# Kernel optimization log

Measured on AMD Instinct MI355X. Metric: run time of the kernel, lower is better.

The kernel has to match this reference:

```python
import jax, jax.numpy as jnp
import numpy as np

N_NODES = 100000
N_EDGES = 1250000
D = 64
K = 5
EPS = 1e-8


def setup_inputs() -> dict:
    key = jax.random.key(0)
    k1, k2, k3, k4 = jax.random.split(key, 4)
    x = jax.random.normal(k1, (N_NODES, D), dtype=jnp.float32)
    mask = jax.random.normal(k2, (N_NODES, 1), dtype=jnp.float32)
    edge_index = jax.random.randint(k3, (2, N_EDGES), 0, N_NODES, dtype=jnp.int64)
    # orthogonal-ish init for the linear layer (QR of gaussian), gain for tanh = 5/3
    g = jax.random.normal(k4, (D, D), dtype=jnp.float32)
    q, _ = jnp.linalg.qr(g)
    W = (5.0 / 3.0) * q.astype(jnp.float32)
    b = jnp.zeros((D,), dtype=jnp.float32)
    alpha = jnp.float32(0.001)
    return {"x": x, "mask": mask, "edge_index": edge_index, "W": W, "b": b, "alpha": alpha}


def _forward(x, mask, edge_index, W, b, alpha):
    n = x.shape[0]
    # x_fn: Linear + Tanh
    h = jnp.tanh(x @ W.T + b)  # [N, D]
    src = edge_index[0]
    dst = edge_index[1]
    hs = h[src]  # [E, D] gather
    hd = h[dst]  # [E, D] gather
    # torch cosine_similarity with eps clamp on each norm
    ns = jnp.maximum(jnp.sqrt(jnp.sum(hs * hs, axis=-1)), EPS)
    nd = jnp.maximum(jnp.sqrt(jnp.sum(hd * hd, axis=-1)), EPS)
    cos = jnp.sum(hs * hd, axis=-1) / (ns * nd)
    edge_weights = jax.nn.relu(cos)  # [E]

    # gcn_norm with self loops (PyG APPNP default): D^-1/2 (A + I) D^-1/2
    loop = jnp.arange(n, dtype=src.dtype)
    row = jnp.concatenate([src, loop])
    col = jnp.concatenate([dst, loop])
    w = jnp.concatenate([edge_weights, jnp.ones((n,), dtype=edge_weights.dtype)])
    deg = jax.ops.segment_sum(w, col, num_segments=n)
    dis = jnp.where(deg > 0, jax.lax.rsqrt(jnp.maximum(deg, EPS)), 0.0)
    norm_w = dis[row] * w * dis[col]  # [E + N]

    # APPNP: K steps of f = (1-alpha) * A_hat @ f + alpha * f0
    f0 = jax.nn.relu(mask)  # [N, 1]
    f = f0
    for _ in range(K):
        msg = norm_w[:, None] * f[row]  # gather + weight
        agg = jax.ops.segment_sum(msg, col, num_segments=n)  # scatter-add
        f = (1.0 - alpha) * agg + alpha * f0
    return f, edge_weights


def reference(x, mask, edge_index, W, b, alpha):
    return _forward(x, mask, edge_index, W, b, alpha)
```

## Files before the change

kernel.cpp:

```cpp
#include <hip/hip_runtime.h>
#include <hip/hip_fp16.h>
#include <math.h>

#define N_NODES 100000
#define N_EDGES 1250000
#define D 64
#define EPS 1e-8f

#define ZERO_BLOCKS 391
#define GEMM_BLOCKS 1024
#define NODE_BLOCKS 391
#define COSR_BLOCKS 9766

__global__ __launch_bounds__(256) void k_gemm_zero(
    const float* __restrict__ x, const float* __restrict__ W,
    const float* __restrict__ b, __half* __restrict__ hn, int* __restrict__ cnt)
{
    if (blockIdx.x < ZERO_BLOCKS) {
        int i = blockIdx.x * 256 + threadIdx.x;
        if (i < N_NODES) cnt[i] = 0;
        return;
    }
    __shared__ float xrow[4][72];
    const int lane = threadIdx.x & 63;
    const int wid  = threadIdx.x >> 6;

    float Wreg[64];
    const float4* Wv = (const float4*)(W + lane * D);
    #pragma unroll
    for (int q = 0; q < 16; ++q) {
        float4 w4 = Wv[q];
        Wreg[4*q+0] = w4.x; Wreg[4*q+1] = w4.y;
        Wreg[4*q+2] = w4.z; Wreg[4*q+3] = w4.w;
    }
    const float bj = b[lane];
    float* xl = xrow[wid];

    const int wave   = (blockIdx.x - ZERO_BLOCKS) * 4 + wid;
    const int nwaves = GEMM_BLOCKS * 4;

    for (int row = wave; row < N_NODES; row += nwaves) {
        float xv = x[(size_t)row * D + lane];
        xl[lane] = xv;
        float acc = bj;
        #pragma unroll
        for (int q = 0; q < 16; ++q) {
            float4 xk4 = *(const float4*)(xl + 4*q);
            acc = fmaf(xk4.x, Wreg[4*q+0], acc);
            acc = fmaf(xk4.y, Wreg[4*q+1], acc);
            acc = fmaf(xk4.z, Wreg[4*q+2], acc);
            acc = fmaf(xk4.w, Wreg[4*q+3], acc);
        }
        float h = tanhf(acc);
        float s = h * h;
        #pragma unroll
        for (int m = 32; m >= 1; m >>= 1) s += __shfl_xor(s, m, 64);
        float nrm = fmaxf(sqrtf(s), EPS);
        hn[(size_t)row * D + lane] = __float2half_rn(h / nrm);
    }
}

__device__ __forceinline__ float dot8h(float4 a, float4 c)
{
    const __half2* ah = (const __half2*)&a;
    const __half2* ch = (const __half2*)&c;
    float p = 0.0f;
    #pragma unroll
    for (int q = 0; q < 4; ++q) {
        float2 af = __half22float2(ah[q]);
        float2 cf = __half22float2(ch[q]);
        p = fmaf(af.x, cf.x, p);
        p = fmaf(af.y, cf.y, p);
    }
    return p;
}

__global__ __launch_bounds__(256) void k_cos_rank(
    const int* __restrict__ ei, const __half* __restrict__ hn,
    int* __restrict__ cnt, int* __restrict__ rank, float* __restrict__ wout)
{
    int t = blockIdx.x * 256 + threadIdx.x;
    int g = t >> 3, sub = t & 7;
    if (g >= N_EDGES / 4) return;
    int e0 = g * 4;
    int4 ss = *(const int4*)(ei + e0);
    int4 dd = *(const int4*)(ei + N_EDGES + e0);

    float4 a0 = ((const float4*)(hn + (size_t)ss.x * D))[sub];
    float4 c0 = ((const float4*)(hn + (size_t)dd.x * D))[sub];
    float4 a1 = ((const float4*)(hn + (size_t)ss.y * D))[sub];
    float4 c1 = ((const float4*)(hn + (size_t)dd.y * D))[sub];
    float4 a2 = ((const float4*)(hn + (size_t)ss.z * D))[sub];
    float4 c2 = ((const float4*)(hn + (size_t)dd.z * D))[sub];
    float4 a3 = ((const float4*)(hn + (size_t)ss.w * D))[sub];
    float4 c3 = ((const float4*)(hn + (size_t)dd.w * D))[sub];

    float p0 = dot8h(a0, c0);
    float p1 = dot8h(a1, c1);
    float p2 = dot8h(a2, c2);
    float p3 = dot8h(a3, c3);
    p0 += __shfl_xor(p0, 1, 64);  p1 += __shfl_xor(p1, 1, 64);
    p2 += __shfl_xor(p2, 1, 64);  p3 += __shfl_xor(p3, 1, 64);
    p0 += __shfl_xor(p0, 2, 64);  p1 += __shfl_xor(p1, 2, 64);
    p2 += __shfl_xor(p2, 2, 64);  p3 += __shfl_xor(p3, 2, 64);
    p0 += __shfl_xor(p0, 4, 64);  p1 += __shfl_xor(p1, 4, 64);
    p2 += __shfl_xor(p2, 4, 64);  p3 += __shfl_xor(p3, 4, 64);

    float w0 = fmaxf(p0, 0.0f);
    float w1 = fmaxf(p1, 0.0f);
    float w2 = fmaxf(p2, 0.0f);
    float w3 = fmaxf(p3, 0.0f);

    if (sub == 0) {
        *(float4*)(wout + e0) = make_float4(w0, w1, w2, w3);
    }
    if (sub < 4) {
        float w = (sub == 0) ? w0 : (sub == 1) ? w1 : (sub == 2) ? w2 : w3;
        int   d = (sub == 0) ? dd.x : (sub == 1) ? dd.y : (sub == 2) ? dd.z : dd.w;
        if (w > 0.0f)
            rank[e0 + sub] = atomicAdd(cnt + d, 1);
    }
}

__device__ __forceinline__ int wave_iscan(int v, int lane)
{
    int incl = v;
    #pragma unroll
    for (int m = 1; m < 64; m <<= 1) {
        int o = __shfl_up(incl, m, 64);
        if (lane >= m) incl += o;
    }
    return incl;
}

__global__ __launch_bounds__(256) void k_scan1(
    const int* __restrict__ cnt, int* __restrict__ rowptr, int* __restrict__ bsum)
{
    __shared__ int wsum[4];
    int t = threadIdx.x, b = blockIdx.x;
    int i = b * 256 + t;
    int lane = t & 63, wid = t >> 6;
    int v = (i < N_NODES) ? cnt[i] : 0;
    int incl = wave_iscan(v, lane);
    if (lane == 63) wsum[wid] = incl;
    __syncthreads();
    int off = 0;
    #pragma unroll
    for (int k = 0; k < 4; ++k) if (k < wid) off += wsum[k];
    if (i < N_NODES) rowptr[i] = off + incl - v;
    if (t == 255) bsum[b] = off + incl;
}

__global__ __launch_bounds__(512) void k_scan2(
    const int* __restrict__ bsum, int* __restrict__ boff, int nblk,
    int* __restrict__ rowptr)
{
    __shared__ int wsum[8];
    int t = threadIdx.x;
    int lane = t & 63, wid = t >> 6;
    int v = (t < nblk) ? bsum[t] : 0;
    int incl = wave_iscan(v, lane);
    if (lane == 63) wsum[wid] = incl;
    __syncthreads();
    int off = 0;
    #pragma unroll
    for (int k = 0; k < 8; ++k) if (k < wid) off += wsum[k];
    if (t < nblk) boff[t] = off + incl - v;
    if (t == nblk - 1) rowptr[N_NODES] = off + incl;
}

__global__ __launch_bounds__(256) void k_place(
    const int* __restrict__ ei, const int* __restrict__ rank_pos,
    const int* __restrict__ rowptr, const int* __restrict__ boff,
    const float* __restrict__ wsrc, int2* __restrict__ pairs)
{
    int e = blockIdx.x * 256 + threadIdx.x;
    if (e >= N_EDGES) return;
    float w = wsrc[e];
    if (!(w > 0.0f)) return;
    int s = ei[e];
    int d = ei[N_EDGES + e];
    int pos = rowptr[d] + boff[d >> 8] + rank_pos[e];
    pairs[pos] = make_int2(s, __float_as_int(w));
}

__global__ __launch_bounds__(256) void k_dis_y(
    const int* __restrict__ rowptr, const int* __restrict__ boff,
    const int2* __restrict__ pairs, const float* __restrict__ mask,
    float* __restrict__ dis, float* __restrict__ y)
{
    int t = blockIdx.x * 256 + threadIdx.x;
    int node = t >> 2, l = t & 3;
    if (node >= N_NODES) return;
    int beg = rowptr[node] + boff[node >> 8];
    int np1 = node + 1;
    int end = rowptr[np1] + (np1 < N_NODES ? boff[np1 >> 8] : 0);
    float s = 0.0f;
    for (int j = beg + l; j < end; j += 8) {
        int2 p0 = pairs[j];
        int j2 = j + 4;
        int2 p1 = make_int2(0, 0);
        if (j2 < end) p1 = pairs[j2];
        s += __int_as_float(p0.y);
        s += __int_as_float(p1.y);
    }
    s += __shfl_xor(s, 1, 64);
    s += __shfl_xor(s, 2, 64);
    if (l == 0) {
        float di = rsqrtf(fmaxf(s + 1.0f, EPS));
        dis[node] = di;
        y[node] = di * fmaxf(mask[node], 0.0f);
    }
}

__global__ __launch_bounds__(256) void k_spmv(
    const int* __restrict__ rowptr, const int* __restrict__ boff,
    const int2* __restrict__ pairs,
    const float* __restrict__ y_in, const float* __restrict__ dis,
    const float* __restrict__ mask, const float* __restrict__ alpha_p,
    float* __restrict__ y_out, float* __restrict__ f_out)
{
    int t = blockIdx.x * 256 + threadIdx.x;
    int node = t >> 2, l = t & 3;
    if (node >= N_NODES) return;
    int beg = rowptr[node] + boff[node >> 8];
    int np1 = node + 1;
    int end = rowptr[np1] + (np1 < N_NODES ? boff[np1 >> 8] : 0);
    float sum = 0.0f;
    for (int j = beg + l; j < end; j += 8) {
        int2 p0 = pairs[j];
        int j2 = j + 4;
        int2 p1 = make_int2(0, 0);
        if (j2 < end) p1 = pairs[j2];
        sum += __int_as_float(p0.y) * y_in[p0.x];
        sum += __int_as_float(p1.y) * y_in[p1.x];
    }
    sum += __shfl_xor(sum, 1, 64);
    sum += __shfl_xor(sum, 2, 64);
    if (l == 0) {
        float di = dis[node];
        float alpha = alpha_p[0];
        float f0 = fmaxf(mask[node], 0.0f);
        float fn = (1.0f - alpha) * di * (sum + y_in[node]) + alpha * f0;
        if (f_out) f_out[node] = fn;
        y_out[node] = di * fn;
    }
}

extern "C" void kernel_launch(void* const* d_in, const int* in_sizes, int n_in,
                              void* d_out, int out_size, void* d_ws, size_t ws_size,
                              hipStream_t stream)
{
    const float* x     = (const float*)d_in[0];
    const float* mask  = (const float*)d_in[1];
    const int*   ei    = (const int*)  d_in[2];
    const float* W     = (const float*)d_in[3];
    const float* b     = (const float*)d_in[4];
    const float* alpha = (const float*)d_in[5];

    float* out_f = (float*)d_out;
    float* out_w = (float*)d_out + N_NODES;

    float* ws = (float*)d_ws;
    __half* hn     = (__half*)ws;
    int2*  pairs   = (int2*) (ws + 3200000);
    int*   rank    = (int*)  (ws + 5700000);
    int*   cnt     = (int*)  (ws + 6950000);
    int*   rowptr  = (int*)  (ws + 7050000);
    float* dis     =          ws + 7150016;
    float* y_a     =          ws + 7250016;
    float* y_b     =          ws + 7350016;
    int*   bsum    = (int*)  (ws + 7550016);
    int*   boff    = (int*)  (ws + 7550528);

    const int edgeBlocks = (N_EDGES + 255) / 256;
    const int segBlocks  = (int)(((long long)N_NODES * 4 + 255) / 256);

    k_gemm_zero<<<ZERO_BLOCKS + GEMM_BLOCKS, 256, 0, stream>>>(x, W, b, hn, cnt);
    k_cos_rank<<<COSR_BLOCKS, 256, 0, stream>>>(ei, hn, cnt, rank, out_w);
    k_scan1<<<NODE_BLOCKS, 256, 0, stream>>>(cnt, rowptr, bsum);
    k_scan2<<<1, 512, 0, stream>>>(bsum, boff, NODE_BLOCKS, rowptr);
    k_place<<<edgeBlocks, 256, 0, stream>>>(ei, rank, rowptr, boff, out_w, pairs);
    k_dis_y<<<segBlocks, 256, 0, stream>>>(rowptr, boff, pairs, mask, dis, y_a);

    k_spmv<<<segBlocks, 256, 0, stream>>>(rowptr, boff, pairs, y_a, dis, mask, alpha, y_b, (float*)nullptr);
    k_spmv<<<segBlocks, 256, 0, stream>>>(rowptr, boff, pairs, y_b, dis, mask, alpha, y_a, (float*)nullptr);
    k_spmv<<<segBlocks, 256, 0, stream>>>(rowptr, boff, pairs, y_a, dis, mask, alpha, y_b, (float*)nullptr);
    k_spmv<<<segBlocks, 256, 0, stream>>>(rowptr, boff, pairs, y_b, dis, mask, alpha, y_a, (float*)nullptr);
    k_spmv<<<segBlocks, 256, 0, stream>>>(rowptr, boff, pairs, y_a, dis, mask, alpha, y_b, out_f);
}
```

Baseline: 208.1 us.

## Fuse scan passes via last-block ticket, widen edge kernels, precompute row descriptors

The two scan kernels become one: the last block to finish, found with an atomic ticket, computes the block offsets. The cosine/rank kernel handles 8 edges per 8-lane group, so every lane issues an atomic and half as many blocks launch. The place kernel processes two edges per thread. Row begin/end pairs are stored once in k_dis_y so the five SpMV passes read one int2 per node instead of rowptr plus boff lookups. This cuts a launch and some index arithmetic, at the cost of more registers per thread and a serial tail in the last scan block.

```diff
diff --git a/kernel.cpp b/kernel.cpp
--- a/kernel.cpp
+++ b/kernel.cpp
@@ -10,15 +10,18 @@
 #define ZERO_BLOCKS 391
 #define GEMM_BLOCKS 1024
 #define NODE_BLOCKS 391
-#define COSR_BLOCKS 9766
+#define COSR_BLOCKS 4883
+#define HALF_EDGES  625000
 
 __global__ __launch_bounds__(256) void k_gemm_zero(
     const float* __restrict__ x, const float* __restrict__ W,
-    const float* __restrict__ b, __half* __restrict__ hn, int* __restrict__ cnt)
+    const float* __restrict__ b, __half* __restrict__ hn,
+    int* __restrict__ cnt, int* __restrict__ ticket)
 {
     if (blockIdx.x < ZERO_BLOCKS) {
         int i = blockIdx.x * 256 + threadIdx.x;
         if (i < N_NODES) cnt[i] = 0;
+        if (blockIdx.x == 0 && threadIdx.x == 0) *ticket = 0;
         return;
     }
     __shared__ float xrow[4][72];
@@ -81,45 +84,64 @@
 {
     int t = blockIdx.x * 256 + threadIdx.x;
     int g = t >> 3, sub = t & 7;
-    if (g >= N_EDGES / 4) return;
-    int e0 = g * 4;
-    int4 ss = *(const int4*)(ei + e0);
-    int4 dd = *(const int4*)(ei + N_EDGES + e0);
-
-    float4 a0 = ((const float4*)(hn + (size_t)ss.x * D))[sub];
-    float4 c0 = ((const float4*)(hn + (size_t)dd.x * D))[sub];
-    float4 a1 = ((const float4*)(hn + (size_t)ss.y * D))[sub];
-    float4 c1 = ((const float4*)(hn + (size_t)dd.y * D))[sub];
-    float4 a2 = ((const float4*)(hn + (size_t)ss.z * D))[sub];
-    float4 c2 = ((const float4*)(hn + (size_t)dd.z * D))[sub];
-    float4 a3 = ((const float4*)(hn + (size_t)ss.w * D))[sub];
-    float4 c3 = ((const float4*)(hn + (size_t)dd.w * D))[sub];
+    if (g >= N_EDGES / 8) return;
+    int e0 = g * 8;
+    int4 ssA = *(const int4*)(ei + e0);
+    int4 ssB = *(const int4*)(ei + e0 + 4);
+    int4 ddA = *(const int4*)(ei + N_EDGES + e0);
+    int4 ddB = *(const int4*)(ei + N_EDGES + e0 + 4);
+
+    float4 a0 = ((const float4*)(hn + (size_t)ssA.x * D))[sub];
+    float4 c0 = ((const float4*)(hn + (size_t)ddA.x * D))[sub];
+    float4 a1 = ((const float4*)(hn + (size_t)ssA.y * D))[sub];
+    float4 c1 = ((const float4*)(hn + (size_t)ddA.y * D))[sub];
+    float4 a2 = ((const float4*)(hn + (size_t)ssA.z * D))[sub];
+    float4 c2 = ((const float4*)(hn + (size_t)ddA.z * D))[sub];
+    float4 a3 = ((const float4*)(hn + (size_t)ssA.w * D))[sub];
+    float4 c3 = ((const float4*)(hn + (size_t)ddA.w * D))[sub];
+    float4 a4 = ((const float4*)(hn + (size_t)ssB.x * D))[sub];
+    float4 c4 = ((const float4*)(hn + (size_t)ddB.x * D))[sub];
+    float4 a5 = ((const float4*)(hn + (size_t)ssB.y * D))[sub];
+    float4 c5 = ((const float4*)(hn + (size_t)ddB.y * D))[sub];
+    float4 a6 = ((const float4*)(hn + (size_t)ssB.z * D))[sub];
+    float4 c6 = ((const float4*)(hn + (size_t)ddB.z * D))[sub];
+    float4 a7 = ((const float4*)(hn + (size_t)ssB.w * D))[sub];
+    float4 c7 = ((const float4*)(hn + (size_t)ddB.w * D))[sub];
 
     float p0 = dot8h(a0, c0);
     float p1 = dot8h(a1, c1);
     float p2 = dot8h(a2, c2);
     float p3 = dot8h(a3, c3);
-    p0 += __shfl_xor(p0, 1, 64);  p1 += __shfl_xor(p1, 1, 64);
-    p2 += __shfl_xor(p2, 1, 64);  p3 += __shfl_xor(p3, 1, 64);
-    p0 += __shfl_xor(p0, 2, 64);  p1 += __shfl_xor(p1, 2, 64);
-    p2 += __shfl_xor(p2, 2, 64);  p3 += __shfl_xor(p3, 2, 64);
-    p0 += __shfl_xor(p0, 4, 64);  p1 += __shfl_xor(p1, 4, 64);
-    p2 += __shfl_xor(p2, 4, 64);  p3 += __shfl_xor(p3, 4, 64);
-
-    float w0 = fmaxf(p0, 0.0f);
-    float w1 = fmaxf(p1, 0.0f);
-    float w2 = fmaxf(p2, 0.0f);
-    float w3 = fmaxf(p3, 0.0f);
-
-    if (sub == 0) {
+    float p4 = dot8h(a4, c4);
+    float p5 = dot8h(a5, c5);
+    float p6 = dot8h(a6, c6);
+    float p7 = dot8h(a7, c7);
+    #pragma unroll
+    for (int m = 1; m <= 4; m <<= 1) {
+        p0 += __shfl_xor(p0, m, 64);  p1 += __shfl_xor(p1, m, 64);
+        p2 += __shfl_xor(p2, m, 64);  p3 += __shfl_xor(p3, m, 64);
+        p4 += __shfl_xor(p4, m, 64);  p5 += __shfl_xor(p5, m, 64);
+        p6 += __shfl_xor(p6, m, 64);  p7 += __shfl_xor(p7, m, 64);
+    }
+
+    float w0 = fmaxf(p0, 0.0f), w1 = fmaxf(p1, 0.0f);
+    float w2 = fmaxf(p2, 0.0f), w3 = fmaxf(p3, 0.0f);
+    float w4 = fmaxf(p4, 0.0f), w5 = fmaxf(p5, 0.0f);
+    float w6 = fmaxf(p6, 0.0f), w7 = fmaxf(p7, 0.0f);
+
+    if (sub == 0)
         *(float4*)(wout + e0) = make_float4(w0, w1, w2, w3);
-    }
-    if (sub < 4) {
-        float w = (sub == 0) ? w0 : (sub == 1) ? w1 : (sub == 2) ? w2 : w3;
-        int   d = (sub == 0) ? dd.x : (sub == 1) ? dd.y : (sub == 2) ? dd.z : dd.w;
-        if (w > 0.0f)
-            rank[e0 + sub] = atomicAdd(cnt + d, 1);
-    }
+    else if (sub == 4)
+        *(float4*)(wout + e0 + 4) = make_float4(w4, w5, w6, w7);
+
+    float w = (sub == 0) ? w0 : (sub == 1) ? w1 : (sub == 2) ? w2 :
+              (sub == 3) ? w3 : (sub == 4) ? w4 : (sub == 5) ? w5 :
+              (sub == 6) ? w6 : w7;
+    int   d = (sub == 0) ? ddA.x : (sub == 1) ? ddA.y : (sub == 2) ? ddA.z :
+              (sub == 3) ? ddA.w : (sub == 4) ? ddB.x : (sub == 5) ? ddB.y :
+              (sub == 6) ? ddB.z : ddB.w;
+    if (w > 0.0f)
+        rank[e0 + sub] = atomicAdd(cnt + d, 1);
 }
 
 __device__ __forceinline__ int wave_iscan(int v, int lane)
@@ -133,10 +155,13 @@
     return incl;
 }
 
-__global__ __launch_bounds__(256) void k_scan1(
-    const int* __restrict__ cnt, int* __restrict__ rowptr, int* __restrict__ bsum)
+__global__ __launch_bounds__(256) void k_scan(
+    const int* __restrict__ cnt, int* __restrict__ rowptr,
+    int* __restrict__ bsum, int* __restrict__ boff, int* __restrict__ ticket)
 {
     __shared__ int wsum[4];
+    __shared__ int amlast;
+    __shared__ int btot;
     int t = threadIdx.x, b = blockIdx.x;
     int i = b * 256 + t;
     int lane = t & 63, wid = t >> 6;
@@ -149,24 +174,28 @@
     for (int k = 0; k < 4; ++k) if (k < wid) off += wsum[k];
     if (i < N_NODES) rowptr[i] = off + incl - v;
     if (t == 255) bsum[b] = off + incl;
-}
-
-__global__ __launch_bounds__(512) void k_scan2(
-    const int* __restrict__ bsum, int* __restrict__ boff, int nblk,
-    int* __restrict__ rowptr)
-{
-    __shared__ int wsum[8];
-    int t = threadIdx.x;
-    int lane = t & 63, wid = t >> 6;
-    int v = (t < nblk) ? bsum[t] : 0;
-    int incl = wave_iscan(v, lane);
-    if (lane == 63) wsum[wid] = incl;
+    __threadfence();
+    if (t == 0) amlast = (atomicAdd(ticket, 1) == gridDim.x - 1);
     __syncthreads();
-    int off = 0;
-    #pragma unroll
-    for (int k = 0; k < 8; ++k) if (k < wid) off += wsum[k];
-    if (t < nblk) boff[t] = off + incl - v;
-    if (t == nblk - 1) rowptr[N_NODES] = off + incl;
+    if (!amlast) return;
+
+    int carry = 0;
+    for (int base = 0; base < NODE_BLOCKS; base += 256) {
+        __syncthreads();
+        int ii = base + t;
+        int vv = (ii < NODE_BLOCKS) ? atomicAdd(&bsum[ii], 0) : 0;
+        int incl2 = wave_iscan(vv, lane);
+        if (lane == 63) wsum[wid] = incl2;
+        __syncthreads();
+        int off2 = 0;
+        #pragma unroll
+        for (int k = 0; k < 4; ++k) if (k < wid) off2 += wsum[k];
+        if (ii < NODE_BLOCKS) boff[ii] = carry + off2 + incl2 - vv;
+        if (t == 255) btot = off2 + incl2;
+        __syncthreads();
+        carry += btot;
+    }
+    if (t == 0) rowptr[N_NODES] = carry;
 }
 
 __global__ __launch_bounds__(256) void k_place(
@@ -175,19 +204,27 @@
     const float* __restrict__ wsrc, int2* __restrict__ pairs)
 {
     int e = blockIdx.x * 256 + threadIdx.x;
-    if (e >= N_EDGES) return;
-    float w = wsrc[e];
-    if (!(w > 0.0f)) return;
-    int s = ei[e];
-    int d = ei[N_EDGES + e];
-    int pos = rowptr[d] + boff[d >> 8] + rank_pos[e];
-    pairs[pos] = make_int2(s, __float_as_int(w));
+    if (e >= HALF_EDGES) return;
+    int e2 = e + HALF_EDGES;
+
+    float wA = wsrc[e];
+    float wB = wsrc[e2];
+    int dA = ei[N_EDGES + e];
+    int dB = ei[N_EDGES + e2];
+    if (wA > 0.0f) {
+        int pos = rowptr[dA] + boff[dA >> 8] + rank_pos[e];
+        pairs[pos] = make_int2(ei[e], __float_as_int(wA));
+    }
+    if (wB > 0.0f) {
+        int pos = rowptr[dB] + boff[dB >> 8] + rank_pos[e2];
+        pairs[pos] = make_int2(ei[e2], __float_as_int(wB));
+    }
 }
 
 __global__ __launch_bounds__(256) void k_dis_y(
     const int* __restrict__ rowptr, const int* __restrict__ boff,
     const int2* __restrict__ pairs, const float* __restrict__ mask,
-    float* __restrict__ dis, float* __restrict__ y)
+    float* __restrict__ dis, float* __restrict__ y, int2* __restrict__ rowdesc)
 {
     int t = blockIdx.x * 256 + threadIdx.x;
     int node = t >> 2, l = t & 3;
@@ -207,6 +244,7 @@
     s += __shfl_xor(s, 1, 64);
     s += __shfl_xor(s, 2, 64);
     if (l == 0) {
+        rowdesc[node] = make_int2(beg, end);
         float di = rsqrtf(fmaxf(s + 1.0f, EPS));
         dis[node] = di;
         y[node] = di * fmaxf(mask[node], 0.0f);
@@ -214,8 +252,7 @@
 }
 
 __global__ __launch_bounds__(256) void k_spmv(
-    const int* __restrict__ rowptr, const int* __restrict__ boff,
-    const int2* __restrict__ pairs,
+    const int2* __restrict__ rowdesc, const int2* __restrict__ pairs,
     const float* __restrict__ y_in, const float* __restrict__ dis,
     const float* __restrict__ mask, const float* __restrict__ alpha_p,
     float* __restrict__ y_out, float* __restrict__ f_out)
@@ -223,15 +260,13 @@
     int t = blockIdx.x * 256 + threadIdx.x;
     int node = t >> 2, l = t & 3;
     if (node >= N_NODES) return;
-    int beg = rowptr[node] + boff[node >> 8];
-    int np1 = node + 1;
-    int end = rowptr[np1] + (np1 < N_NODES ? boff[np1 >> 8] : 0);
+    int2 rd = rowdesc[node];
     float sum = 0.0f;
-    for (int j = beg + l; j < end; j += 8) {
+    for (int j = rd.x + l; j < rd.y; j += 8) {
         int2 p0 = pairs[j];
         int j2 = j + 4;
         int2 p1 = make_int2(0, 0);
-        if (j2 < end) p1 = pairs[j2];
+        if (j2 < rd.y) p1 = pairs[j2];
         sum += __int_as_float(p0.y) * y_in[p0.x];
         sum += __int_as_float(p1.y) * y_in[p1.x];
     }
@@ -270,22 +305,23 @@
     float* dis     =          ws + 7150016;
     float* y_a     =          ws + 7250016;
     float* y_b     =          ws + 7350016;
-    int*   bsum    = (int*)  (ws + 7550016);
-    int*   boff    = (int*)  (ws + 7550528);
-
-    const int edgeBlocks = (N_EDGES + 255) / 256;
-    const int segBlocks  = (int)(((long long)N_NODES * 4 + 255) / 256);
-
-    k_gemm_zero<<<ZERO_BLOCKS + GEMM_BLOCKS, 256, 0, stream>>>(x, W, b, hn, cnt);
+    int2*  rowdesc = (int2*) (ws + 7450016);
+    int*   bsum    = (int*)  (ws + 7650016);
+    int*   boff    = (int*)  (ws + 7650528);
+    int*   ticket  = (int*)  (ws + 7651040);
+
+    const int placeBlocks = (HALF_EDGES + 255) / 256;
+    const int segBlocks   = (int)(((long long)N_NODES * 4 + 255) / 256);
+
+    k_gemm_zero<<<ZERO_BLOCKS + GEMM_BLOCKS, 256, 0, stream>>>(x, W, b, hn, cnt, ticket);
     k_cos_rank<<<COSR_BLOCKS, 256, 0, stream>>>(ei, hn, cnt, rank, out_w);
-    k_scan1<<<NODE_BLOCKS, 256, 0, stream>>>(cnt, rowptr, bsum);
-    k_scan2<<<1, 512, 0, stream>>>(bsum, boff, NODE_BLOCKS, rowptr);
-    k_place<<<edgeBlocks, 256, 0, stream>>>(ei, rank, rowptr, boff, out_w, pairs);
-    k_dis_y<<<segBlocks, 256, 0, stream>>>(rowptr, boff, pairs, mask, dis, y_a);
-
-    k_spmv<<<segBlocks, 256, 0, stream>>>(rowptr, boff, pairs, y_a, dis, mask, alpha, y_b, (float*)nullptr);
-    k_spmv<<<segBlocks, 256, 0, stream>>>(rowptr, boff, pairs, y_b, dis, mask, alpha, y_a, (float*)nullptr);
-    k_spmv<<<segBlocks, 256, 0, stream>>>(rowptr, boff, pairs, y_a, dis, mask, alpha, y_b, (float*)nullptr);
-    k_spmv<<<segBlocks, 256, 0, stream>>>(rowptr, boff, pairs, y_b, dis, mask, alpha, y_a, (float*)nullptr);
-    k_spmv<<<segBlocks, 256, 0, stream>>>(rowptr, boff, pairs, y_a, dis, mask, alpha, y_b, out_f);
-}
+    k_scan<<<NODE_BLOCKS, 256, 0, stream>>>(cnt, rowptr, bsum, boff, ticket);
+    k_place<<<placeBlocks, 256, 0, stream>>>(ei, rank, rowptr, boff, out_w, pairs);
+    k_dis_y<<<segBlocks, 256, 0, stream>>>(rowptr, boff, pairs, mask, dis, y_a, rowdesc);
+
+    k_spmv<<<segBlocks, 256, 0, stream>>>(rowdesc, pairs, y_a, dis, mask, alpha, y_b, (float*)nullptr);
+    k_spmv<<<segBlocks, 256, 0, stream>>>(rowdesc, pairs, y_b, dis, mask, alpha, y_a, (float*)nullptr);
+    k_spmv<<<segBlocks, 256, 0, stream>>>(rowdesc, pairs, y_a, dis, mask, alpha, y_b, (float*)nullptr);
+    k_spmv<<<segBlocks, 256, 0, stream>>>(rowdesc, pairs, y_b, dis, mask, alpha, y_a, (float*)nullptr);
+    k_spmv<<<segBlocks, 256, 0, stream>>>(rowdesc, pairs, y_a, dis, mask, alpha, y_b, out_f);
+}
```

Measured after the change: 232.1 us. 11.5% more time.
